# Performance work log

Measured on AMD Instinct MI355X. Metric: run time of the kernel, lower is better.

Reference implementation:

```python
import jax, jax.numpy as jnp
import numpy as np

# Module hyperparameters (from init_kwargs)
KERNEL = (16, 16)     # sliding window shape; Linear in_features = prod = 256
STRIDE = (8, 8)       # window stride
DILATION = (4, 4)     # per-window output tile; Linear out_features = prod = 16
# padding = 0, bias = False (module defaults)


def setup_inputs() -> dict:
    key = jax.random.key(0)
    k1, k2 = jax.random.split(key)
    x = jax.random.normal(k1, (32, 1024, 1024), dtype=jnp.float32)
    # torch nn.Linear weight convention: [out_features, in_features] = [16, 256]
    weight = jax.random.normal(k2, (16, 256), dtype=jnp.float32) / 16.0  # ~1/sqrt(in)
    return {"x": x, "weight": weight}


def reference(x, weight):
    # im2col: extract all sliding windows, flattened in (kh, kw) row-major order
    # (matches torch's window.flatten() since there is a single implicit channel).
    B = x.shape[0]
    patches = jax.lax.conv_general_dilated_patches(
        x[:, None],                 # [B, 1, H, W]
        filter_shape=KERNEL,
        window_strides=STRIDE,
        padding='VALID',
    )                               # [B, prod(KERNEL)=256, nH=127, nW=127]
    nH, nW = patches.shape[2], patches.shape[3]
    d0, d1 = DILATION
    # Dense per-patch linear: y = W @ flat_window   (bias=False)
    out = jnp.einsum('bkij,ok->bijo', patches, weight)   # [B, nH, nW, 16]
    # Each patch's 16 outputs reshape to a (4,4) tile placed at its output site.
    out = out.reshape(B, nH, nW, d0, d1)
    out = out.transpose(0, 1, 3, 2, 4).reshape(B, nH * d0, nW * d1)  # [B, 508, 508]
    return out
```

## Files before the change

kernel.cpp:

```cpp
#include <hip/hip_runtime.h>


typedef __attribute__((ext_vector_type(8))) short short8;
typedef __attribute__((ext_vector_type(4))) float f32x4;

#define ROWS   40
#define ROWG   72
#define ROWE   (ROWG * 8)
#define NG8    (ROWS * 65)

__device__ __forceinline__ unsigned short f2bf(float f) {
    unsigned int u = __builtin_bit_cast(unsigned int, f);
    u = (u + 0x7fffu + ((u >> 16) & 1u)) >> 16;
    return (unsigned short)u;
}

__global__ __launch_bounds__(256, 3)
void conv_mfma2(const float* __restrict__ x,
                const float* __restrict__ w,
                float* __restrict__ out) {
    __shared__ unsigned short lds[ROWS * ROWE];

    const int tid  = threadIdx.x;
    const int lane = tid & 63;
    const int wv   = tid >> 6;
    const int bx   = blockIdx.x;
    const int h    = bx & 1;
    const int i0   = (bx >> 1) * 4;
    const int b    = blockIdx.y;

    const float* xb = x + (size_t)b * (1024 * 1024);
    const int basecol = h * 504;
    const int jb      = h * 63;

    const int o = lane & 15;
    short8 wfrag[8];
    #pragma unroll
    for (int s = 0; s < 8; ++s) {
        const float* wp = w + o * 256 + s * 32 + (lane >> 4) * 8;
        float4 w0 = *(const float4*)wp;
        float4 w1 = *(const float4*)(wp + 4);
        short8 f;
        f[0] = (short)f2bf(w0.x); f[1] = (short)f2bf(w0.y);
        f[2] = (short)f2bf(w0.z); f[3] = (short)f2bf(w0.w);
        f[4] = (short)f2bf(w1.x); f[5] = (short)f2bf(w1.y);
        f[6] = (short)f2bf(w1.z); f[7] = (short)f2bf(w1.w);
        wfrag[s] = f;
    }

    for (int it = 0; it < 11; ++it) {
        int g8 = tid + it * 256;
        if (g8 < NG8) {
            int row = g8 / 65;
            int c8  = g8 - row * 65;
            int grow = i0 * 8 + row; if (grow > 1023) grow = 1023;
            const float* src = xb + grow * 1024 + basecol + c8 * 8;
            float4 v0 = *(const float4*)src;
            float4 v1 = *(const float4*)(src + 4);
            short8 hh;
            hh[0] = (short)f2bf(v0.x); hh[1] = (short)f2bf(v0.y);
            hh[2] = (short)f2bf(v0.z); hh[3] = (short)f2bf(v0.w);
            hh[4] = (short)f2bf(v1.x); hh[5] = (short)f2bf(v1.y);
            hh[6] = (short)f2bf(v1.z); hh[7] = (short)f2bf(v1.w);
            int slot = c8 ^ (row & 7);
            *(short8*)&lds[row * ROWE + slot * 8] = hh;
        }
    }
    __syncthreads();

    const int m  = lane & 15;
    const int kb = (lane >> 4) & 1;
    const int hi = lane >> 5;
    const int ip = i0 + wv;
    const int p  = lane >> 4;

    #pragma unroll
    for (int jt = 0; jt < 4; ++jt) {
        const int gl = jt * 16 + m + kb;
        f32x4 acc = {0.f, 0.f, 0.f, 0.f};
        #pragma unroll
        for (int s = 0; s < 8; ++s) {
            int row  = wv * 8 + 2 * s + hi;
            int slot = gl ^ (row & 7);
            short8 a = *(const short8*)&lds[row * ROWE + slot * 8];
            acc = __builtin_amdgcn_mfma_f32_16x16x32_bf16(wfrag[s], a, acc, 0, 0, 0);
        }
        if (ip < 127) {
            const int jp = jb + jt * 16 + m;
            float* op = out + (size_t)b * (508 * 508) + (ip * 4 + p) * 508 + jp * 4;
            *(float4*)op = *(float4*)&acc;
        }
    }
}

extern "C" void kernel_launch(void* const* d_in, const int* in_sizes, int n_in,
                              void* d_out, int out_size, void* d_ws, size_t ws_size,
                              hipStream_t stream) {
    const float* x = (const float*)d_in[0];
    const float* w = (const float*)d_in[1];
    float* out = (float*)d_out;
    dim3 grid(64, 32);
    conv_mfma2<<<grid, dim3(256, 1, 1), 0, stream>>>(x, w, out);
}
```

Before: 43.75 us.

## Retile to 8 patch-rows by quarter-width per block with 512 threads and packed bf16 conversion

Each block now covers 8 patch rows across a quarter of the width (32 patch columns), using 8 waves instead of 4 patch rows across half the width. The LDS layout becomes an odd-stride (33) array of 16-byte groups in place of the XOR swizzle, which spreads bank conflicts while making the addresses simpler. fp32→bf16 conversion switches to the hardware v_cvt_pk_bf16_f32 instruction. The vertical halo overhead drops (72 rows loaded per 8 patch rows instead of 40 per 4), though the horizontal halo grows and blocks are larger, which may limit occupancy.

Result: slower. 48.47 us (+10.8%).

```diff
diff --git a/kernel.cpp b/kernel.cpp
--- a/kernel.cpp
+++ b/kernel.cpp
@@ -4,34 +4,33 @@
 typedef __attribute__((ext_vector_type(8))) short short8;
 typedef __attribute__((ext_vector_type(4))) float f32x4;
 
-#define ROWS   40
-#define ROWG   72
-#define ROWE   (ROWG * 8)
-#define NG8    (ROWS * 65)
+#define ROWS 72
+#define ROWG 33
+#define NG   (ROWS * ROWG)
 
-__device__ __forceinline__ unsigned short f2bf(float f) {
-    unsigned int u = __builtin_bit_cast(unsigned int, f);
-    u = (u + 0x7fffu + ((u >> 16) & 1u)) >> 16;
-    return (unsigned short)u;
+__device__ __forceinline__ unsigned pk2(float a, float b) {
+    unsigned r;
+    asm("v_cvt_pk_bf16_f32 %0, %1, %2" : "=v"(r) : "v"(a), "v"(b));
+    return r;
 }
 
-__global__ __launch_bounds__(256, 3)
-void conv_mfma2(const float* __restrict__ x,
+__global__ __launch_bounds__(512, 4)
+void conv_mfma3(const float* __restrict__ x,
                 const float* __restrict__ w,
                 float* __restrict__ out) {
-    __shared__ unsigned short lds[ROWS * ROWE];
+    __shared__ uint4 lds[NG];
 
     const int tid  = threadIdx.x;
     const int lane = tid & 63;
     const int wv   = tid >> 6;
     const int bx   = blockIdx.x;
-    const int h    = bx & 1;
-    const int i0   = (bx >> 1) * 4;
+    const int st   = bx & 3;
+    const int i0   = (bx >> 2) * 8;
     const int b    = blockIdx.y;
 
     const float* xb = x + (size_t)b * (1024 * 1024);
-    const int basecol = h * 504;
-    const int jb      = h * 63;
+    const int basecol = st * 256;
+    const int jb      = st * 32;
 
     const int o = lane & 15;
     short8 wfrag[8];
@@ -40,53 +39,41 @@
         const float* wp = w + o * 256 + s * 32 + (lane >> 4) * 8;
         float4 w0 = *(const float4*)wp;
         float4 w1 = *(const float4*)(wp + 4);
-        short8 f;
-        f[0] = (short)f2bf(w0.x); f[1] = (short)f2bf(w0.y);
-        f[2] = (short)f2bf(w0.z); f[3] = (short)f2bf(w0.w);
-        f[4] = (short)f2bf(w1.x); f[5] = (short)f2bf(w1.y);
-        f[6] = (short)f2bf(w1.z); f[7] = (short)f2bf(w1.w);
-        wfrag[s] = f;
+        uint4 f = make_uint4(pk2(w0.x, w0.y), pk2(w0.z, w0.w),
+                             pk2(w1.x, w1.y), pk2(w1.z, w1.w));
+        wfrag[s] = __builtin_bit_cast(short8, f);
     }
 
-    for (int it = 0; it < 11; ++it) {
-        int g8 = tid + it * 256;
-        if (g8 < NG8) {
-            int row = g8 / 65;
-            int c8  = g8 - row * 65;
-            int grow = i0 * 8 + row; if (grow > 1023) grow = 1023;
-            const float* src = xb + grow * 1024 + basecol + c8 * 8;
-            float4 v0 = *(const float4*)src;
-            float4 v1 = *(const float4*)(src + 4);
-            short8 hh;
-            hh[0] = (short)f2bf(v0.x); hh[1] = (short)f2bf(v0.y);
-            hh[2] = (short)f2bf(v0.z); hh[3] = (short)f2bf(v0.w);
-            hh[4] = (short)f2bf(v1.x); hh[5] = (short)f2bf(v1.y);
-            hh[6] = (short)f2bf(v1.z); hh[7] = (short)f2bf(v1.w);
-            int slot = c8 ^ (row & 7);
-            *(short8*)&lds[row * ROWE + slot * 8] = hh;
-        }
+    for (int g = tid; g < NG; g += 512) {
+        int row = g / ROWG;
+        int c8  = g - row * ROWG;
+        int grow = i0 * 8 + row;      if (grow > 1023) grow = 1023;
+        int gcol = basecol + c8 * 8;  if (gcol > 1016) gcol = 1016;
+        const float* src = xb + grow * 1024 + gcol;
+        float4 v0 = *(const float4*)src;
+        float4 v1 = *(const float4*)(src + 4);
+        lds[g] = make_uint4(pk2(v0.x, v0.y), pk2(v0.z, v0.w),
+                            pk2(v1.x, v1.y), pk2(v1.z, v1.w));
     }
     __syncthreads();
 
     const int m  = lane & 15;
     const int kb = (lane >> 4) & 1;
     const int hi = lane >> 5;
+    const int p  = lane >> 4;
     const int ip = i0 + wv;
-    const int p  = lane >> 4;
+    const int g0 = (wv * 8 + hi) * ROWG + m + kb;
 
     #pragma unroll
-    for (int jt = 0; jt < 4; ++jt) {
-        const int gl = jt * 16 + m + kb;
+    for (int jt = 0; jt < 2; ++jt) {
         f32x4 acc = {0.f, 0.f, 0.f, 0.f};
         #pragma unroll
         for (int s = 0; s < 8; ++s) {
-            int row  = wv * 8 + 2 * s + hi;
-            int slot = gl ^ (row & 7);
-            short8 a = *(const short8*)&lds[row * ROWE + slot * 8];
+            short8 a = *(const short8*)&lds[g0 + s * (2 * ROWG) + jt * 16];
             acc = __builtin_amdgcn_mfma_f32_16x16x32_bf16(wfrag[s], a, acc, 0, 0, 0);
         }
-        if (ip < 127) {
-            const int jp = jb + jt * 16 + m;
+        const int jp = jb + jt * 16 + m;
+        if (ip < 127 && jp < 127) {
             float* op = out + (size_t)b * (508 * 508) + (ip * 4 + p) * 508 + jp * 4;
             *(float4*)op = *(float4*)&acc;
         }
@@ -100,5 +87,5 @@
     const float* w = (const float*)d_in[1];
     float* out = (float*)d_out;
     dim3 grid(64, 32);
-    conv_mfma2<<<grid, dim3(256, 1, 1), 0, stream>>>(x, w, out);
+    conv_mfma3<<<grid, dim3(512, 1, 1), 0, stream>>>(x, w, out);
 }
```
